# Performance work log

Hardware: AMD Instinct MI355X
Metric: run time of the kernel (lower is better)

Reference implementation:

```python
import jax, jax.numpy as jnp
import numpy as np

# Static problem sizes (uniform ragged batch -> dense-packable)
B, NC, NP, C = 16, 128, 256, 128
HID = 2 * C            # mlp_hidden_scale * embedding_channels
COORD_SCALE = 5.0      # args.coord_scale
DIS_THRES = 10.0       # args.dis_map_thres
N_PROT = 16384         # total protein_whole residues
MAXN = 2 + NC + NP     # per-sample complex length (glb_c + compound + glb_p + pocket)


def setup_inputs() -> dict:
    key = jax.random.key(0)
    ks = jax.random.split(key, 12)
    protein_feats = jax.random.normal(ks[0], (N_PROT, 1280), jnp.float32)
    compound_feats = jax.random.normal(ks[1], (B * NC, 56), jnp.float32)
    complex_coords = jax.random.normal(ks[2], (B * MAXN, 3), jnp.float32) * 10.0
    dis_map = jax.random.uniform(ks[3], (B * NP * NC,), jnp.float32) * DIS_THRES
    keep_idx = jnp.sort(jax.random.randint(ks[4], (B * NP,), 0, N_PROT))
    glb_c = jnp.ones((1, C), jnp.float32)
    glb_p = jnp.ones((1, C), jnp.float32)
    # xavier_uniform with gain=0.001 ~ tiny weights
    W_prot = jax.random.normal(ks[5], (1280, C), jnp.float32) * 0.001
    b_prot = jnp.zeros((C,), jnp.float32)
    W_comp = jax.random.normal(ks[6], (56, C), jnp.float32) * 0.001
    b_comp = jnp.zeros((C,), jnp.float32)
    W1 = jax.random.normal(ks[7], (C, HID), jnp.float32) / np.sqrt(C)
    b1 = jnp.zeros((HID,), jnp.float32)
    W2 = jax.random.normal(ks[8], (HID, 1), jnp.float32) / np.sqrt(HID)
    b2 = jnp.zeros((1,), jnp.float32)
    return dict(protein_feats=protein_feats, compound_feats=compound_feats,
                complex_coords=complex_coords, dis_map=dis_map, keep_idx=keep_idx,
                glb_c=glb_c, glb_p=glb_p, W_prot=W_prot, b_prot=b_prot,
                W_comp=W_comp, b_comp=b_comp, W1=W1, b1=b1, W2=W2, b2=b2)


def reference(protein_feats, compound_feats, complex_coords, dis_map, keep_idx,
              glb_c, glb_p, W_prot, b_prot, W_comp, b_comp, W1, b1, W2, b2):
    # --- input projections + keepNode gather (pocket residues from whole protein)
    pocket_emb = (protein_feats[keep_idx] @ W_prot + b_prot).reshape(B, NP, C)
    compound_emb = (compound_feats @ W_comp + b_comp).reshape(B, NC, C)

    # --- ragged batch assembly: per-sample [glb_c, compound_i, glb_p, pocket_i]
    # (uniform sizes -> single dense concat replaces the Python loop of mask+cat)
    gc = jnp.broadcast_to(glb_c[None], (B, 1, C))
    gp = jnp.broadcast_to(glb_p[None], (B, 1, C))
    new_samples = jnp.concatenate([gc, compound_emb, gp, pocket_emb], axis=1)  # [B, MAXN, C]

    # --- stand-in pair embedding for EfficientMCAttModel output:
    # pair_embed_batched[b, i, j] over (glb_p+pocket) x (glb_c+compound)
    p_side = new_samples[:, NC + 1:, :]     # [B, NP+1, C]
    c_side = new_samples[:, :NC + 1, :]     # [B, NC+1, C]
    pair = p_side[:, :, None, :] + c_side[:, None, :, :]  # [B, NP+1, NC+1, C]

    # --- coordinates (normalize, split by segment/is_global layout)
    coords = (complex_coords / COORD_SCALE).reshape(B, MAXN, 3)
    compound_coords_n = coords[:, 1:NC + 1, :]   # [B, NC, 3]
    pocket_coords_n = coords[:, NC + 2:, :]      # [B, NP, 3]

    # --- cdist(pocket, compound)  [B, NP, NC]
    diff = pocket_coords_n[:, :, None, :] - compound_coords_n[:, None, :, :]
    dmap = jnp.sqrt(jnp.sum(diff * diff, axis=-1) + 1e-12)

    # --- distmap MLP on z = pair[:, 1:, 1:] then sigmoid * thres
    z = pair[:, 1:, 1:, :]                        # [B, NP, NC, C]
    h = jax.nn.relu(z @ W1 + b1)                  # [B, NP, NC, HID]
    logits = (h @ W2 + b2)[..., 0]                # [B, NP, NC]
    # z_mask = outer(pocket_mask, compound_mask) is all-True for uniform sizes
    y_pred = jax.nn.sigmoid(logits).reshape(-1) * DIS_THRES
    y_pred_by_coords = jnp.clip(dmap.reshape(-1) * COORD_SCALE, 0.0, DIS_THRES)

    compound_coords_out = compound_coords_n.reshape(-1, 3) * COORD_SCALE
    pocket_coords_out = pocket_coords_n.reshape(-1, 3) * COORD_SCALE
    compound_batch = jnp.repeat(jnp.arange(B, dtype=jnp.int32), NC)
    pocket_batch = jnp.repeat(jnp.arange(B, dtype=jnp.int32), NP)
    keepNode_less_5 = jnp.zeros((), jnp.int32)
    return (compound_coords_out, compound_batch, pocket_coords_out, pocket_batch,
            y_pred, y_pred_by_coords, dis_map, keepNode_less_5)
```

## Files before the change

kernel.cpp:

```cpp
#include <hip/hip_runtime.h>
#include <hip/hip_bf16.h>
#include <cstddef>


typedef __attribute__((ext_vector_type(8))) short short8v;
typedef __attribute__((ext_vector_type(4))) float f32x4;
typedef _Float16 half2v __attribute__((ext_vector_type(2)));
typedef _Float16 half8v __attribute__((ext_vector_type(8)));

__device__ __forceinline__ unsigned int f2bf(float x) {
    unsigned int u = __float_as_uint(x);
    return (u + 0x7fffu + ((u >> 16) & 1u)) >> 16;
}

__device__ __forceinline__ float dot8h(half8v r, half8v w, float acc) {
#if __has_builtin(__builtin_amdgcn_fdot2)
#pragma unroll
    for (int q = 0; q < 4; ++q) {
        half2v rq = {r[2 * q], r[2 * q + 1]};
        half2v wq = {w[2 * q], w[2 * q + 1]};
        acc = __builtin_amdgcn_fdot2(rq, wq, acc, false);
    }
#else
#pragma unroll
    for (int q = 0; q < 8; ++q) acc += (float)r[q] * (float)w[q];
#endif
    return acc;
}

#define WS_WTP   0u
#define WS_WTC   655360u
#define WS_BP1   688128u
#define WS_BC1   689152u
#define WS_W2H   690176u
#define WS_P1H   691200u
#define WS_PPH   3836928u

__global__ __launch_bounds__(256) void k_fusew(const float* __restrict__ Wp,
                                               const float* __restrict__ Wc,
                                               const float* __restrict__ bp,
                                               const float* __restrict__ bc,
                                               const float* __restrict__ W1,
                                               const float* __restrict__ b1,
                                               const float* __restrict__ W2,
                                               const float* __restrict__ coords,
                                               const float* __restrict__ dism,
                                               float* __restrict__ out,
                                               char* __restrict__ ws) {
    const int tid = threadIdx.x, bid = blockIdx.x;

    if (bid >= 336) {
        const int g = (bid - 336) * 256 + tid;
        {
            const float4* src = reinterpret_cast<const float4*>(dism + (size_t)g * 8);
            float4* dst = reinterpret_cast<float4*>(out + 1073152 + (size_t)g * 8);
            dst[0] = src[0]; dst[1] = src[1];
        }
        if (g < 6144) {
            const int row = g / 3, d = g - row * 3;
            const int bb2 = row >> 7, c = row & 127;
            const float x = coords[(size_t)(bb2 * 386 + 1 + c) * 3 + d];
            out[g] = (x / 5.0f) * 5.0f;
        }
        if (g < 2048) out[6144 + g] = (float)(g >> 7);
        if (g < 12288) {
            const int row = g / 3, d = g - row * 3;
            const int bb2 = row >> 8, p = row & 255;
            const float x = coords[(size_t)(bb2 * 386 + 130 + p) * 3 + d];
            out[8192 + g] = (x / 5.0f) * 5.0f;
        }
        if (g < 4096) out[20480 + g] = (float)(g >> 8);
        if (g == 0) out[1597440] = 0.0f;
        return;
    }

    __shared__ float Al[8][128];
    const int wb = bid >> 1, nh = bid & 1;
    const int row0 = wb * 8;
    {
        const int r = tid >> 5, k4 = (tid & 31) * 4;
        const int rg = row0 + r;
        float4 v = make_float4(0.f, 0.f, 0.f, 0.f);
        if (rg < 1280)       v = *reinterpret_cast<const float4*>(Wp + (size_t)rg * 128 + k4);
        else if (rg < 1336)  v = *reinterpret_cast<const float4*>(Wc + (size_t)(rg - 1280) * 128 + k4);
        else if (rg == 1336) v = *reinterpret_cast<const float4*>(bp + k4);
        else if (rg == 1337) v = *reinterpret_cast<const float4*>(bc + k4);
        *reinterpret_cast<float4*>(&Al[r][k4]) = v;
    }
    __syncthreads();
    const int col = (tid & 127) + nh * 128;
    const int rh = tid >> 7;
    float acc[4] = {0.f, 0.f, 0.f, 0.f};
#pragma unroll 4
    for (int k4 = 0; k4 < 128; k4 += 4) {
        float w0 = W1[(k4 + 0) * 256 + col];
        float w1 = W1[(k4 + 1) * 256 + col];
        float w2 = W1[(k4 + 2) * 256 + col];
        float w3 = W1[(k4 + 3) * 256 + col];
#pragma unroll
        for (int r = 0; r < 4; ++r) {
            float4 a = *reinterpret_cast<const float4*>(&Al[rh * 4 + r][k4]);
            acc[r] += a.x * w0 + a.y * w1 + a.z * w2 + a.w * w3;
        }
    }
    if (wb < 160) {
        const unsigned int w0 = f2bf(acc[0]) | (f2bf(acc[1]) << 16);
        const unsigned int w1 = f2bf(acc[2]) | (f2bf(acc[3]) << 16);
        unsigned short* WtP = (unsigned short*)(ws + WS_WTP);
        *reinterpret_cast<uint2*>(WtP + (size_t)col * 1280 + row0 + rh * 4) = make_uint2(w0, w1);
    } else if (wb < 167) {
        const unsigned int w0 = f2bf(acc[0]) | (f2bf(acc[1]) << 16);
        const unsigned int w1 = f2bf(acc[2]) | (f2bf(acc[3]) << 16);
        unsigned short* WtC = (unsigned short*)(ws + WS_WTC);
        *reinterpret_cast<uint2*>(WtC + (size_t)col * 64 + (row0 - 1280) + rh * 4) = make_uint2(w0, w1);
    } else {
        if (rh == 0) {
            ((float*)(ws + WS_BP1))[col] = acc[0] + b1[col];
            ((float*)(ws + WS_BC1))[col] = acc[1];
        } else {
            ((_Float16*)(ws + WS_W2H))[col] = (_Float16)W2[col];
            unsigned short* WtC = (unsigned short*)(ws + WS_WTC);
            *reinterpret_cast<uint2*>(WtC + (size_t)col * 64 + 56) = make_uint2(0, 0);
            *reinterpret_cast<uint2*>(WtC + (size_t)col * 64 + 60) = make_uint2(0, 0);
        }
    }
}

struct AB { float4 ra[2]; uint4 rb[4]; };

__device__ __forceinline__ void load_tile(AB& t, bool pocket, int koff, int nh,
                                          const float* __restrict__ prot,
                                          const float* __restrict__ comp,
                                          const int* keepL, int m0,
                                          const unsigned short* __restrict__ Bt,
                                          int bstride, int tid) {
#pragma unroll
    for (int u = 0; u < 2; ++u) {
        const int unit = tid + 256 * u;
        const int r = unit >> 4, kc = unit & 15;
        float4 v = make_float4(0.f, 0.f, 0.f, 0.f);
        if (pocket) {
            v = *reinterpret_cast<const float4*>(prot + (size_t)keepL[r] * 1280 + koff + kc * 4);
        } else if (kc < 14) {
            v = *reinterpret_cast<const float4*>(comp + (size_t)(m0 + r - 4096) * 56 + kc * 4);
        }
        t.ra[u] = v;
    }
#pragma unroll
    for (int u = 0; u < 4; ++u) {
        const int unit = tid + 256 * u;
        const int col = unit >> 3, k8 = unit & 7;
        t.rb[u] = *reinterpret_cast<const uint4*>(Bt + (size_t)(nh * 128 + col) * bstride + koff + k8 * 8);
    }
}

__device__ __forceinline__ void store_tile(const AB& t, char* As, char* Bs, int tid) {
#pragma unroll
    for (int u = 0; u < 2; ++u) {
        const int unit = tid + 256 * u;
        const int r = unit >> 4, kc = unit & 15;
        const float4 v = t.ra[u];
        const unsigned int lo = f2bf(v.x) | (f2bf(v.y) << 16);
        const unsigned int hi = f2bf(v.z) | (f2bf(v.w) << 16);
        const int wb = (r * 128 + kc * 8) ^ ((r & 7) << 4);
        *reinterpret_cast<uint2*>(As + wb) = make_uint2(lo, hi);
    }
#pragma unroll
    for (int u = 0; u < 4; ++u) {
        const int unit = tid + 256 * u;
        const int col = unit >> 3, k8 = unit & 7;
        const int wb = (col * 128 + k8 * 16) ^ ((col & 7) << 4);
        *reinterpret_cast<uint4*>(Bs + wb) = t.rb[u];
    }
}

__global__ __launch_bounds__(256) void k_gemm(const float* __restrict__ prot,
                                              const int* __restrict__ keep,
                                              const float* __restrict__ comp,
                                              char* __restrict__ ws) {
    __shared__ __align__(16) char As[32 * 64 * 2];
    __shared__ __align__(16) char Bs[128 * 64 * 2];
    __shared__ int keepL[32];
    const int tid = threadIdx.x;
    const int l = tid & 63, wn = tid >> 6;
    const int l15 = l & 15, lg = l >> 4;
    const int bid = blockIdx.x;
    const bool pocket = (bid < 1024);
    int m0, ks, nh, iters, koff0, bstride;
    const unsigned short* Bt;
    if (pocket) {
        const int a = bid & 7, c = bid >> 4;
        nh = (bid >> 3) & 1;
        const int tile = a + (c << 3);
        m0 = (tile >> 2) * 32;
        ks = tile & 3;
        koff0 = ks * 320; iters = 5;
        Bt = (const unsigned short*)(ws + WS_WTP); bstride = 1280;
    } else {
        const int u = bid - 1024;
        m0 = 4096 + (u >> 1) * 32;
        nh = u & 1; ks = 0;
        koff0 = 0; iters = 1;
        Bt = (const unsigned short*)(ws + WS_WTC); bstride = 64;
    }

    if (pocket && tid < 32) keepL[tid] = keep[m0 + tid];
    __syncthreads();

    f32x4 acc[2][2];
#pragma unroll
    for (int m = 0; m < 2; ++m)
#pragma unroll
        for (int n = 0; n < 2; ++n) acc[m][n] = (f32x4){0.f, 0.f, 0.f, 0.f};

    AB cur, nxt;
    load_tile(cur, pocket, koff0, nh, prot, comp, keepL, m0, Bt, bstride, tid);

    for (int it = 0; it < iters; ++it) {
        if (it) __syncthreads();
        store_tile(cur, As, Bs, tid);
        __syncthreads();
        if (it + 1 < iters)
            load_tile(nxt, pocket, koff0 + (it + 1) * 64, nh, prot, comp, keepL, m0, Bt, bstride, tid);
#pragma unroll
        for (int kstep = 0; kstep < 2; ++kstep) {
            const int kbyte = kstep * 64 + lg * 16;
            short8v a[2], b[2];
#pragma unroll
            for (int m = 0; m < 2; ++m) {
                const int row = m * 16 + l15;
                a[m] = *reinterpret_cast<const short8v*>(As + ((row * 128 + kbyte) ^ ((row & 7) << 4)));
            }
#pragma unroll
            for (int n = 0; n < 2; ++n) {
                const int col = wn * 32 + n * 16 + l15;
                b[n] = *reinterpret_cast<const short8v*>(Bs + ((col * 128 + kbyte) ^ ((col & 7) << 4)));
            }
#pragma unroll
            for (int m = 0; m < 2; ++m)
#pragma unroll
                for (int n = 0; n < 2; ++n)
                    acc[m][n] = __builtin_amdgcn_mfma_f32_16x16x32_bf16(a[m], b[n], acc[m][n], 0, 0, 0);
        }
        if (it + 1 < iters) cur = nxt;
    }

    if (pocket) {
        _Float16* dst = (_Float16*)(ws + WS_PPH + (size_t)ks * 2097152u);
        const float* bias = (const float*)(ws + WS_BP1);
#pragma unroll
        for (int m = 0; m < 2; ++m)
#pragma unroll
            for (int n = 0; n < 2; ++n) {
                const int col = nh * 128 + wn * 32 + n * 16 + l15;
                const float bb = (ks == 0) ? bias[col] : 0.f;
#pragma unroll
                for (int i = 0; i < 4; ++i) {
                    const int row = m0 + m * 16 + lg * 4 + i;
                    dst[((size_t)row << 8) + col] = (_Float16)(acc[m][n][i] + bb);
                }
            }
    } else {
        const float* bias = (const float*)(ws + WS_BC1);
        _Float16* P1h = (_Float16*)(ws + WS_P1H);
#pragma unroll
        for (int m = 0; m < 2; ++m)
#pragma unroll
            for (int n = 0; n < 2; ++n) {
                const int col = nh * 128 + wn * 32 + n * 16 + l15;
                const float bb = bias[col];
#pragma unroll
                for (int i = 0; i < 4; ++i) {
                    const int row = m0 + m * 16 + lg * 4 + i;
                    P1h[(size_t)row * 256 + col] = (_Float16)(acc[m][n][i] + bb);
                }
            }
    }
}

__global__ __launch_bounds__(256) void k_pair(const char* __restrict__ ws,
                                              const float* __restrict__ b2,
                                              const float* __restrict__ coords,
                                              float* __restrict__ out) {
    __shared__ __align__(16) char Ph[32 * 512];
    __shared__ __align__(16) char Ch[32 * 512];
    __shared__ __align__(16) _Float16 W2l[256];
    __shared__ float pcs[32][3], ccs[32][3];
    const int tid = threadIdx.x;
    const int b = blockIdx.z, p0 = blockIdx.y * 32, c0 = blockIdx.x * 32;
    const _Float16* P1h = (const _Float16*)(ws + WS_P1H);
    const _Float16* pp = (const _Float16*)(ws + WS_PPH);

#pragma unroll
    for (int u = 0; u < 4; ++u) {
        const int unit = tid + 256 * u;
        const int row = unit >> 5, h8 = unit & 31;
        const size_t base = (((size_t)(b * 256 + p0 + row)) << 8) + h8 * 8;
        const half8v s0 = *reinterpret_cast<const half8v*>(pp + base);
        const half8v s1 = *reinterpret_cast<const half8v*>(pp + 1048576u + base);
        const half8v s2 = *reinterpret_cast<const half8v*>(pp + 2097152u + base);
        const half8v s3 = *reinterpret_cast<const half8v*>(pp + 3145728u + base);
        const half8v t = (s0 + s1) + (s2 + s3);
        const int key = ((row ^ (row >> 2)) & 7) << 4;
        *reinterpret_cast<half8v*>(Ph + ((row * 512 + h8 * 16) ^ key)) = t;
    }
#pragma unroll
    for (int u = 0; u < 4; ++u) {
        const int unit = tid + 256 * u;
        const int row = unit >> 5, h8 = unit & 31;
        const uint4 v = *reinterpret_cast<const uint4*>(P1h + (size_t)(4096 + b * 128 + c0 + row) * 256 + h8 * 8);
        const int key = ((row ^ (row >> 2)) & 7) << 4;
        *reinterpret_cast<uint4*>(Ch + ((row * 512 + h8 * 16) ^ key)) = v;
    }
    if (tid < 32) {
        *reinterpret_cast<uint4*>(W2l + tid * 8) =
            *reinterpret_cast<const uint4*>((const _Float16*)(ws + WS_W2H) + tid * 8);
        const float* s = coords + (size_t)(b * 386 + 130 + p0 + tid) * 3;
        pcs[tid][0] = s[0] / 5.0f; pcs[tid][1] = s[1] / 5.0f; pcs[tid][2] = s[2] / 5.0f;
    } else if (tid < 64) {
        const int t = tid - 32;
        const float* s = coords + (size_t)(b * 386 + 1 + c0 + t) * 3;
        ccs[t][0] = s[0] / 5.0f; ccs[t][1] = s[1] / 5.0f; ccs[t][2] = s[2] / 5.0f;
    }
    __syncthreads();

    const int pi = tid >> 4, ci = tid & 15;
    float acc[2][2] = {{0.f, 0.f}, {0.f, 0.f}};
#pragma unroll 4
    for (int h8 = 0; h8 < 32; ++h8) {
        const half8v wv = *reinterpret_cast<const half8v*>((const char*)W2l + h8 * 16);
        half8v pf[2], cf[2];
#pragma unroll
        for (int i = 0; i < 2; ++i) {
            const int row = pi * 2 + i;
            const int key = ((row ^ (row >> 2)) & 7) << 4;
            pf[i] = *reinterpret_cast<const half8v*>(Ph + ((row * 512 + h8 * 16) ^ key));
        }
#pragma unroll
        for (int j = 0; j < 2; ++j) {
            const int row = ci * 2 + j;
            const int key = ((row ^ (row >> 2)) & 7) << 4;
            cf[j] = *reinterpret_cast<const half8v*>(Ch + ((row * 512 + h8 * 16) ^ key));
        }
#pragma unroll
        for (int i = 0; i < 2; ++i)
#pragma unroll
            for (int j = 0; j < 2; ++j) {
                half8v s = pf[i] + cf[j];
                half8v r = __builtin_elementwise_max(s, (half8v)0);
                acc[i][j] = dot8h(r, wv, acc[i][j]);
            }
    }

    const float bb = b2[0];
#pragma unroll
    for (int i = 0; i < 2; ++i) {
        const int pr = pi * 2 + i;
        float2 y2, yc2;
        float* yp = &y2.x; float* yq = &yc2.x;
#pragma unroll
        for (int j = 0; j < 2; ++j) {
            const int cr = ci * 2 + j;
            const float logit = acc[i][j] + bb;
            yp[j] = 10.0f / (1.0f + expf(-logit));
            const float dx = pcs[pr][0] - ccs[cr][0];
            const float dy = pcs[pr][1] - ccs[cr][1];
            const float dz = pcs[pr][2] - ccs[cr][2];
            const float d = sqrtf(dx * dx + dy * dy + dz * dz + 1e-12f);
            yq[j] = fminf(fmaxf(d * 5.0f, 0.0f), 10.0f);
        }
        const size_t o = (size_t)(b * 256 + p0 + pr) * 128 + c0 + ci * 2;
        *reinterpret_cast<float2*>(out + 24576 + o) = y2;
        *reinterpret_cast<float2*>(out + 548864 + o) = yc2;
    }
}

extern "C" void kernel_launch(void* const* d_in, const int* in_sizes, int n_in,
                              void* d_out, int out_size, void* d_ws, size_t ws_size,
                              hipStream_t stream) {
    const float* prot   = (const float*)d_in[0];
    const float* comp   = (const float*)d_in[1];
    const float* coords = (const float*)d_in[2];
    const float* dism   = (const float*)d_in[3];
    const int*   keep   = (const int*)d_in[4];
    const float* Wp = (const float*)d_in[7];
    const float* bp = (const float*)d_in[8];
    const float* Wc = (const float*)d_in[9];
    const float* bc = (const float*)d_in[10];
    const float* W1 = (const float*)d_in[11];
    const float* b1 = (const float*)d_in[12];
    const float* W2 = (const float*)d_in[13];
    const float* b2 = (const float*)d_in[14];
    float* out = (float*)d_out;
    char* ws = (char*)d_ws;

    k_fusew<<<592, 256, 0, stream>>>(Wp, Wc, bp, bc, W1, b1, W2, coords, dism, out, ws);
    k_gemm<<<1152, 256, 0, stream>>>(prot, keep, comp, ws);
    k_pair<<<dim3(4, 8, 16), 256, 0, stream>>>(ws, b2, coords, out);
}
```

Before: 39.80 us.

## Widen GEMM blocks to full N and enlarge pair-kernel compound tile

The projection GEMM now gives each 512-thread block all 256 output columns instead of splitting N across two blocks. This halves the redundant gathered-row loads of protein features, and a prefetch now runs two tiles ahead. The pair kernel now covers 64 compounds per block with 4 compounds per thread, which reuses the pocket features more and writes float4 outputs. The cost is fewer blocks in both kernels (less parallelism on many CUs), more registers per thread, and more LDS.

Result: no change. 39.28 us (-1.3%).

```diff
diff --git a/kernel.cpp b/kernel.cpp
--- a/kernel.cpp
+++ b/kernel.cpp
@@ -126,40 +126,36 @@
     }
 }
 
-struct AB { float4 ra[2]; uint4 rb[4]; };
-
-__device__ __forceinline__ void load_tile(AB& t, bool pocket, int koff, int nh,
+struct AB { float4 ra; uint4 rb[4]; };
+
+__device__ __forceinline__ void load_tile(AB& t, bool pocket, int koff,
                                           const float* __restrict__ prot,
                                           const float* __restrict__ comp,
                                           const int* keepL, int m0,
                                           const unsigned short* __restrict__ Bt,
                                           int bstride, int tid) {
-#pragma unroll
-    for (int u = 0; u < 2; ++u) {
-        const int unit = tid + 256 * u;
-        const int r = unit >> 4, kc = unit & 15;
+    {
+        const int r = tid >> 4, kc = tid & 15;
         float4 v = make_float4(0.f, 0.f, 0.f, 0.f);
         if (pocket) {
             v = *reinterpret_cast<const float4*>(prot + (size_t)keepL[r] * 1280 + koff + kc * 4);
         } else if (kc < 14) {
             v = *reinterpret_cast<const float4*>(comp + (size_t)(m0 + r - 4096) * 56 + kc * 4);
         }
-        t.ra[u] = v;
+        t.ra = v;
     }
 #pragma unroll
     for (int u = 0; u < 4; ++u) {
-        const int unit = tid + 256 * u;
+        const int unit = tid + 512 * u;
         const int col = unit >> 3, k8 = unit & 7;
-        t.rb[u] = *reinterpret_cast<const uint4*>(Bt + (size_t)(nh * 128 + col) * bstride + koff + k8 * 8);
+        t.rb[u] = *reinterpret_cast<const uint4*>(Bt + (size_t)col * bstride + koff + k8 * 8);
     }
 }
 
 __device__ __forceinline__ void store_tile(const AB& t, char* As, char* Bs, int tid) {
-#pragma unroll
-    for (int u = 0; u < 2; ++u) {
-        const int unit = tid + 256 * u;
-        const int r = unit >> 4, kc = unit & 15;
-        const float4 v = t.ra[u];
+    {
+        const int r = tid >> 4, kc = tid & 15;
+        const float4 v = t.ra;
         const unsigned int lo = f2bf(v.x) | (f2bf(v.y) << 16);
         const unsigned int hi = f2bf(v.z) | (f2bf(v.w) << 16);
         const int wb = (r * 128 + kc * 8) ^ ((r & 7) << 4);
@@ -167,114 +163,103 @@
     }
 #pragma unroll
     for (int u = 0; u < 4; ++u) {
-        const int unit = tid + 256 * u;
+        const int unit = tid + 512 * u;
         const int col = unit >> 3, k8 = unit & 7;
         const int wb = (col * 128 + k8 * 16) ^ ((col & 7) << 4);
         *reinterpret_cast<uint4*>(Bs + wb) = t.rb[u];
     }
 }
 
-__global__ __launch_bounds__(256) void k_gemm(const float* __restrict__ prot,
+__global__ __launch_bounds__(512) void k_gemm(const float* __restrict__ prot,
                                               const int* __restrict__ keep,
                                               const float* __restrict__ comp,
                                               char* __restrict__ ws) {
     __shared__ __align__(16) char As[32 * 64 * 2];
-    __shared__ __align__(16) char Bs[128 * 64 * 2];
+    __shared__ __align__(16) char Bs[256 * 64 * 2];
     __shared__ int keepL[32];
     const int tid = threadIdx.x;
-    const int l = tid & 63, wn = tid >> 6;
+    const int l = tid & 63, wid = tid >> 6;
+    const int wm = wid & 1, wn = wid >> 1;
     const int l15 = l & 15, lg = l >> 4;
     const int bid = blockIdx.x;
-    const bool pocket = (bid < 1024);
-    int m0, ks, nh, iters, koff0, bstride;
+    const bool pocket = (bid < 512);
+    int m0, ks, iters, koff0, bstride;
     const unsigned short* Bt;
     if (pocket) {
-        const int a = bid & 7, c = bid >> 4;
-        nh = (bid >> 3) & 1;
-        const int tile = a + (c << 3);
-        m0 = (tile >> 2) * 32;
-        ks = tile & 3;
+        m0 = (bid >> 2) * 32;
+        ks = bid & 3;
         koff0 = ks * 320; iters = 5;
         Bt = (const unsigned short*)(ws + WS_WTP); bstride = 1280;
     } else {
-        const int u = bid - 1024;
-        m0 = 4096 + (u >> 1) * 32;
-        nh = u & 1; ks = 0;
-        koff0 = 0; iters = 1;
+        m0 = 4096 + (bid - 512) * 32;
+        ks = 0; koff0 = 0; iters = 1;
         Bt = (const unsigned short*)(ws + WS_WTC); bstride = 64;
     }
 
     if (pocket && tid < 32) keepL[tid] = keep[m0 + tid];
     __syncthreads();
 
-    f32x4 acc[2][2];
-#pragma unroll
-    for (int m = 0; m < 2; ++m)
-#pragma unroll
-        for (int n = 0; n < 2; ++n) acc[m][n] = (f32x4){0.f, 0.f, 0.f, 0.f};
-
-    AB cur, nxt;
-    load_tile(cur, pocket, koff0, nh, prot, comp, keepL, m0, Bt, bstride, tid);
+    f32x4 acc[4];
+#pragma unroll
+    for (int n = 0; n < 4; ++n) acc[n] = (f32x4){0.f, 0.f, 0.f, 0.f};
+
+    AB t0, t1, t2;
+    load_tile(t0, pocket, koff0, prot, comp, keepL, m0, Bt, bstride, tid);
+    if (iters > 1)
+        load_tile(t1, pocket, koff0 + 64, prot, comp, keepL, m0, Bt, bstride, tid);
 
     for (int it = 0; it < iters; ++it) {
         if (it) __syncthreads();
-        store_tile(cur, As, Bs, tid);
+        store_tile(t0, As, Bs, tid);
         __syncthreads();
-        if (it + 1 < iters)
-            load_tile(nxt, pocket, koff0 + (it + 1) * 64, nh, prot, comp, keepL, m0, Bt, bstride, tid);
+        if (it + 2 < iters)
+            load_tile(t2, pocket, koff0 + (it + 2) * 64, prot, comp, keepL, m0, Bt, bstride, tid);
 #pragma unroll
         for (int kstep = 0; kstep < 2; ++kstep) {
             const int kbyte = kstep * 64 + lg * 16;
-            short8v a[2], b[2];
-#pragma unroll
-            for (int m = 0; m < 2; ++m) {
-                const int row = m * 16 + l15;
-                a[m] = *reinterpret_cast<const short8v*>(As + ((row * 128 + kbyte) ^ ((row & 7) << 4)));
-            }
-#pragma unroll
-            for (int n = 0; n < 2; ++n) {
-                const int col = wn * 32 + n * 16 + l15;
+            short8v a, b[4];
+            {
+                const int row = wm * 16 + l15;
+                a = *reinterpret_cast<const short8v*>(As + ((row * 128 + kbyte) ^ ((row & 7) << 4)));
+            }
+#pragma unroll
+            for (int n = 0; n < 4; ++n) {
+                const int col = wn * 64 + n * 16 + l15;
                 b[n] = *reinterpret_cast<const short8v*>(Bs + ((col * 128 + kbyte) ^ ((col & 7) << 4)));
             }
 #pragma unroll
-            for (int m = 0; m < 2; ++m)
-#pragma unroll
-                for (int n = 0; n < 2; ++n)
-                    acc[m][n] = __builtin_amdgcn_mfma_f32_16x16x32_bf16(a[m], b[n], acc[m][n], 0, 0, 0);
-        }
-        if (it + 1 < iters) cur = nxt;
+            for (int n = 0; n < 4; ++n)
+                acc[n] = __builtin_amdgcn_mfma_f32_16x16x32_bf16(a, b[n], acc[n], 0, 0, 0);
+        }
+        if (it + 1 < iters) { t0 = t1; t1 = t2; }
     }
 
     if (pocket) {
         _Float16* dst = (_Float16*)(ws + WS_PPH + (size_t)ks * 2097152u);
         const float* bias = (const float*)(ws + WS_BP1);
 #pragma unroll
-        for (int m = 0; m < 2; ++m)
-#pragma unroll
-            for (int n = 0; n < 2; ++n) {
-                const int col = nh * 128 + wn * 32 + n * 16 + l15;
-                const float bb = (ks == 0) ? bias[col] : 0.f;
-#pragma unroll
-                for (int i = 0; i < 4; ++i) {
-                    const int row = m0 + m * 16 + lg * 4 + i;
-                    dst[((size_t)row << 8) + col] = (_Float16)(acc[m][n][i] + bb);
-                }
-            }
+        for (int n = 0; n < 4; ++n) {
+            const int col = wn * 64 + n * 16 + l15;
+            const float bb = (ks == 0) ? bias[col] : 0.f;
+#pragma unroll
+            for (int i = 0; i < 4; ++i) {
+                const int row = m0 + wm * 16 + lg * 4 + i;
+                dst[((size_t)row << 8) + col] = (_Float16)(acc[n][i] + bb);
+            }
+        }
     } else {
         const float* bias = (const float*)(ws + WS_BC1);
         _Float16* P1h = (_Float16*)(ws + WS_P1H);
 #pragma unroll
-        for (int m = 0; m < 2; ++m)
-#pragma unroll
-            for (int n = 0; n < 2; ++n) {
-                const int col = nh * 128 + wn * 32 + n * 16 + l15;
-                const float bb = bias[col];
-#pragma unroll
-                for (int i = 0; i < 4; ++i) {
-                    const int row = m0 + m * 16 + lg * 4 + i;
-                    P1h[(size_t)row * 256 + col] = (_Float16)(acc[m][n][i] + bb);
-                }
-            }
+        for (int n = 0; n < 4; ++n) {
+            const int col = wn * 64 + n * 16 + l15;
+            const float bb = bias[col];
+#pragma unroll
+            for (int i = 0; i < 4; ++i) {
+                const int row = m0 + wm * 16 + lg * 4 + i;
+                P1h[(size_t)row * 256 + col] = (_Float16)(acc[n][i] + bb);
+            }
+        }
     }
 }
 
@@ -283,11 +268,11 @@
                                               const float* __restrict__ coords,
                                               float* __restrict__ out) {
     __shared__ __align__(16) char Ph[32 * 512];
-    __shared__ __align__(16) char Ch[32 * 512];
+    __shared__ __align__(16) char Ch[64 * 512];
     __shared__ __align__(16) _Float16 W2l[256];
-    __shared__ float pcs[32][3], ccs[32][3];
+    __shared__ float pcs[32][3], ccs[64][3];
     const int tid = threadIdx.x;
-    const int b = blockIdx.z, p0 = blockIdx.y * 32, c0 = blockIdx.x * 32;
+    const int b = blockIdx.z, p0 = blockIdx.y * 32, c0 = blockIdx.x * 64;
     const _Float16* P1h = (const _Float16*)(ws + WS_P1H);
     const _Float16* pp = (const _Float16*)(ws + WS_PPH);
 
@@ -305,7 +290,7 @@
         *reinterpret_cast<half8v*>(Ph + ((row * 512 + h8 * 16) ^ key)) = t;
     }
 #pragma unroll
-    for (int u = 0; u < 4; ++u) {
+    for (int u = 0; u < 8; ++u) {
         const int unit = tid + 256 * u;
         const int row = unit >> 5, h8 = unit & 31;
         const uint4 v = *reinterpret_cast<const uint4*>(P1h + (size_t)(4096 + b * 128 + c0 + row) * 256 + h8 * 8);
@@ -317,7 +302,7 @@
             *reinterpret_cast<const uint4*>((const _Float16*)(ws + WS_W2H) + tid * 8);
         const float* s = coords + (size_t)(b * 386 + 130 + p0 + tid) * 3;
         pcs[tid][0] = s[0] / 5.0f; pcs[tid][1] = s[1] / 5.0f; pcs[tid][2] = s[2] / 5.0f;
-    } else if (tid < 64) {
+    } else if (tid < 96) {
         const int t = tid - 32;
         const float* s = coords + (size_t)(b * 386 + 1 + c0 + t) * 3;
         ccs[t][0] = s[0] / 5.0f; ccs[t][1] = s[1] / 5.0f; ccs[t][2] = s[2] / 5.0f;
@@ -325,11 +310,11 @@
     __syncthreads();
 
     const int pi = tid >> 4, ci = tid & 15;
-    float acc[2][2] = {{0.f, 0.f}, {0.f, 0.f}};
+    float acc[2][4] = {{0.f, 0.f, 0.f, 0.f}, {0.f, 0.f, 0.f, 0.f}};
 #pragma unroll 4
     for (int h8 = 0; h8 < 32; ++h8) {
         const half8v wv = *reinterpret_cast<const half8v*>((const char*)W2l + h8 * 16);
-        half8v pf[2], cf[2];
+        half8v pf[2], cf[4];
 #pragma unroll
         for (int i = 0; i < 2; ++i) {
             const int row = pi * 2 + i;
@@ -337,15 +322,15 @@
             pf[i] = *reinterpret_cast<const half8v*>(Ph + ((row * 512 + h8 * 16) ^ key));
         }
 #pragma unroll
-        for (int j = 0; j < 2; ++j) {
-            const int row = ci * 2 + j;
+        for (int j = 0; j < 4; ++j) {
+            const int row = ci * 4 + j;
             const int key = ((row ^ (row >> 2)) & 7) << 4;
             cf[j] = *reinterpret_cast<const half8v*>(Ch + ((row * 512 + h8 * 16) ^ key));
         }
 #pragma unroll
         for (int i = 0; i < 2; ++i)
 #pragma unroll
-            for (int j = 0; j < 2; ++j) {
+            for (int j = 0; j < 4; ++j) {
                 half8v s = pf[i] + cf[j];
                 half8v r = __builtin_elementwise_max(s, (half8v)0);
                 acc[i][j] = dot8h(r, wv, acc[i][j]);
@@ -356,11 +341,11 @@
 #pragma unroll
     for (int i = 0; i < 2; ++i) {
         const int pr = pi * 2 + i;
-        float2 y2, yc2;
-        float* yp = &y2.x; float* yq = &yc2.x;
-#pragma unroll
-        for (int j = 0; j < 2; ++j) {
-            const int cr = ci * 2 + j;
+        float4 y4, yc4;
+        float* yp = &y4.x; float* yq = &yc4.x;
+#pragma unroll
+        for (int j = 0; j < 4; ++j) {
+            const int cr = ci * 4 + j;
             const float logit = acc[i][j] + bb;
             yp[j] = 10.0f / (1.0f + expf(-logit));
             const float dx = pcs[pr][0] - ccs[cr][0];
@@ -369,9 +354,9 @@
             const float d = sqrtf(dx * dx + dy * dy + dz * dz + 1e-12f);
             yq[j] = fminf(fmaxf(d * 5.0f, 0.0f), 10.0f);
         }
-        const size_t o = (size_t)(b * 256 + p0 + pr) * 128 + c0 + ci * 2;
-        *reinterpret_cast<float2*>(out + 24576 + o) = y2;
-        *reinterpret_cast<float2*>(out + 548864 + o) = yc2;
+        const size_t o = (size_t)(b * 256 + p0 + pr) * 128 + c0 + ci * 4;
+        *reinterpret_cast<float4*>(out + 24576 + o) = y4;
+        *reinterpret_cast<float4*>(out + 548864 + o) = yc4;
     }
 }
 
@@ -395,6 +380,6 @@
     char* ws = (char*)d_ws;
 
     k_fusew<<<592, 256, 0, stream>>>(Wp, Wc, bp, bc, W1, b1, W2, coords, dism, out, ws);
-    k_gemm<<<1152, 256, 0, stream>>>(prot, keep, comp, ws);
-    k_pair<<<dim3(4, 8, 16), 256, 0, stream>>>(ws, b2, coords, out);
-}
+    k_gemm<<<576, 512, 0, stream>>>(prot, keep, comp, ws);
+    k_pair<<<dim3(2, 8, 16), 256, 0, stream>>>(ws, b2, coords, out);
+}
```
